# Performance work log

Hardware: AMD Instinct MI355X
Metric: run time of the kernel (lower is better)

The kernel has to match this reference:

```python
import jax, jax.numpy as jnp
import numpy as np

B, S, N = 128, 64, 32          # batch, self nodes, neighbors per node
INP_CAPS, OUT_CAPS, CAP_SZ = 8, 8, 16
K = OUT_CAPS
D = OUT_CAPS * CAP_SZ          # 128
C = D // K                     # capsule dim = 16
TAU = 1.0
EPS = 1e-12                    # F.normalize eps


def _l2norm(x):
    n = jnp.sqrt(jnp.sum(x * x, axis=-1, keepdims=True))
    return x / jnp.maximum(n, EPS)


def setup_inputs() -> dict:
    key = jax.random.key(0)
    k1, k2, k3, k4 = jax.random.split(key, 4)
    inp_d = INP_CAPS * CAP_SZ
    return {
        "self_vectors": jax.random.normal(k1, (B, S, inp_d), dtype=jnp.float32),
        "neighbor_vectors": jax.random.normal(k2, (B, S, N, inp_d), dtype=jnp.float32),
        "w1": jax.random.normal(k3, (inp_d, D), dtype=jnp.float32) * (1.0 / np.sqrt(inp_d)),
        "b1": jax.random.normal(k4, (D,), dtype=jnp.float32) * (1.0 / np.sqrt(D)),
        "max_iter": 3,
    }


def reference(self_vectors, neighbor_vectors, w1, b1, max_iter):
    inp_d = INP_CAPS * CAP_SZ
    self_z = jax.nn.relu(self_vectors.reshape(-1, inp_d) @ w1 + b1)
    neigh_z = jax.nn.relu(neighbor_vectors.reshape(-1, inp_d) @ w1 + b1)

    # [B,S,K,C] and [B,S,N,K,C], each capsule L2-normalized
    self_zn = _l2norm(self_z.reshape(B, S, K, C))
    neigh_zn = _l2norm(neigh_z.reshape(B, S, N, K, C))

    u = None
    for it in range(max_iter):
        if u is None:
            p = jnp.zeros((B, S, N, K), dtype=self_zn.dtype)
        else:
            # agreement scores: [B,S,N,K]
            p = jnp.einsum("bsnkc,bskc->bsnk", neigh_zn, u)
        p = jax.nn.softmax(p / TAU, axis=-1)
        # weighted neighbor sum over N -> [B,S,K,C]
        u = jnp.einsum("bsnkc,bsnk->bskc", neigh_zn, p) + self_zn
        if it < max_iter - 1:
            u = _l2norm(u)

    # dropout p=0.0 (eval) -> identity
    return jax.nn.relu(u.reshape(B, S, D))
```

## Files before the change

### kernel.cpp

```cpp
#include <hip/hip_runtime.h>
#include <hip/hip_bf16.h>


#define NB 32
#define DD 128
#define ZS 132
#define PPS 40
#define AST 136

#define SMEM_BYTES 19232
#define ALO_OFF_SH 4488
#define UU_OFF_F 4352
#define PP_OFF_F 4488

typedef __attribute__((ext_vector_type(8))) short bf16x8;
typedef __attribute__((ext_vector_type(4))) float f32x4;
typedef __attribute__((ext_vector_type(4))) float float4v;
typedef __attribute__((ext_vector_type(2))) unsigned int uint2v;

__device__ __forceinline__ float bf16bits_to_f32(unsigned short u) {
  return __uint_as_float(((unsigned int)u) << 16);
}
__device__ __forceinline__ void split_bf16(float x, unsigned short& hi, unsigned short& lo) {
  unsigned int xb = __float_as_uint(x);
  hi = (unsigned short)(xb >> 16);
  float hif = __uint_as_float(xb & 0xFFFF0000u);
  float lof = x - hif;
  lo = (unsigned short)(__float_as_uint(lof) >> 16);
}

__device__ __forceinline__ void split4_store(float4v v, unsigned short* hp,
                                             unsigned short* lp) {
  unsigned int a = __float_as_uint(v[0]);
  unsigned int b = __float_as_uint(v[1]);
  unsigned int c = __float_as_uint(v[2]);
  unsigned int d = __float_as_uint(v[3]);
  unsigned int h01 = __builtin_amdgcn_perm(b, a, 0x07060302u);
  unsigned int h23 = __builtin_amdgcn_perm(d, c, 0x07060302u);
  unsigned int la = __float_as_uint(v[0] - __uint_as_float(a & 0xFFFF0000u));
  unsigned int lb = __float_as_uint(v[1] - __uint_as_float(b & 0xFFFF0000u));
  unsigned int lc = __float_as_uint(v[2] - __uint_as_float(c & 0xFFFF0000u));
  unsigned int ld = __float_as_uint(v[3] - __uint_as_float(d & 0xFFFF0000u));
  unsigned int l01 = __builtin_amdgcn_perm(lb, la, 0x07060302u);
  unsigned int l23 = __builtin_amdgcn_perm(ld, lc, 0x07060302u);
  *(uint2v*)hp = (uint2v){h01, h23};
  *(uint2v*)lp = (uint2v){l01, l23};
}

__global__ __launch_bounds__(256) void swizzle_w_kernel(
    const void* __restrict__ w1, int* __restrict__ flag,
    unsigned short* __restrict__ whi, unsigned short* __restrict__ wlo) {
  __shared__ int sflag;
  int t = threadIdx.x;
  if (t < 64) {
    float v = bf16bits_to_f32(((const unsigned short*)w1)[2 * t]);
    int hit = !(fabsf(v) < 1e4f);
    unsigned long long m = __ballot(hit);
    if (t == 0) sflag = (m != 0ull) ? 1 : 0;
  }
  __syncthreads();
  const int isf = sflag;
  if (blockIdx.x == 0 && t == 0) *flag = isf;

  int idx = blockIdx.x * 256 + t;
  int k = idx >> 7, n = idx & 127;
  int kt = k >> 5, q = (k >> 3) & 3, j = k & 7;
  int nt = n >> 4, nl = n & 15;
  int lane = q * 16 + nl;
  int dst = ((kt * 8 + nt) * 64 + lane) * 8 + j;
  unsigned short hb, lb;
  if (isf) {
    split_bf16(((const float*)w1)[idx], hb, lb);
  } else {
    hb = ((const unsigned short*)w1)[idx];
    lb = 0;
  }
  whi[dst] = hb;
  wlo[dst] = lb;
}

template <bool OUTF32>
__device__ __forceinline__ void routing_tail(unsigned char* smem, void* out,
                                             size_t bs) {
  float* zn = (float*)smem;
  float* uu = (float*)smem + UU_OFF_F;
  float* pp = (float*)smem + PP_OFF_F;
  const int tid = threadIdx.x;
  const int lane = tid & 63;
  const int wv = tid >> 6;

  {
    const int rowr = (tid & 7) | ((tid >> 6) << 3);
    const int kr = (tid >> 3) & 7;
    float4v* zp = (float4v*)&zn[rowr * ZS + kr * 16];
    float4v a = zp[0], b = zp[1], c = zp[2], d = zp[3];
    float ss = a[0]*a[0]+a[1]*a[1]+a[2]*a[2]+a[3]*a[3]
             + b[0]*b[0]+b[1]*b[1]+b[2]*b[2]+b[3]*b[3]
             + c[0]*c[0]+c[1]*c[1]+c[2]*c[2]+c[3]*c[3]
             + d[0]*d[0]+d[1]*d[1]+d[2]*d[2]+d[3]*d[3];
    float nv = 1.f / fmaxf(sqrtf(ss), 1e-12f);
    zp[0] = a * nv; zp[1] = b * nv; zp[2] = c * nv; zp[3] = d * nv;
  }
  if (tid < 8) {
    float4v* zp = (float4v*)&zn[32 * ZS + tid * 16];
    float4v a = zp[0], b = zp[1], c = zp[2], d = zp[3];
    float ss = a[0]*a[0]+a[1]*a[1]+a[2]*a[2]+a[3]*a[3]
             + b[0]*b[0]+b[1]*b[1]+b[2]*b[2]+b[3]*b[3]
             + c[0]*c[0]+c[1]*c[1]+c[2]*c[2]+c[3]*c[3]
             + d[0]*d[0]+d[1]*d[1]+d[2]*d[2]+d[3]*d[3];
    float nv = 1.f / fmaxf(sqrtf(ss), 1e-12f);
    zp[0] = a * nv; zp[1] = b * nv; zp[2] = c * nv; zp[3] = d * nv;
  }
  __syncthreads();

  const int k2 = tid >> 5, half = (tid >> 4) & 1, c2 = tid & 15;
  const float selfz = zn[32 * ZS + k2 * 16 + c2];
  const int k1 = (lane >> 3) & 7;
  const int n1 = (lane & 7) | (wv << 3);

  {
    float s = 0.f;
#pragma unroll
    for (int n0 = 0; n0 < 16; ++n0)
      s += zn[(half * 16 + n0) * ZS + k2 * 16 + c2];
    s += __shfl_xor(s, 16);
    s = 0.125f * s + selfz;
    float ss = s * s;
    ss += __shfl_xor(ss, 1);
    ss += __shfl_xor(ss, 2);
    ss += __shfl_xor(ss, 4);
    ss += __shfl_xor(ss, 8);
    s *= 1.f / fmaxf(sqrtf(ss), 1e-12f);
    if (half == 0) uu[k2 * 16 + c2] = s;
    __syncthreads();
  }

  for (int it = 1; it < 3; ++it) {
    {
      const float4v* up = (const float4v*)&uu[k1 * 16];
      float4v u0 = up[0], u1 = up[1], u2 = up[2], u3 = up[3];
      const float4v* zp = (const float4v*)&zn[n1 * ZS + k1 * 16];
      float4v z0 = zp[0], z1 = zp[1], z2 = zp[2], z3 = zp[3];
      float logit = u0[0]*z0[0]+u0[1]*z0[1]+u0[2]*z0[2]+u0[3]*z0[3]
                  + u1[0]*z1[0]+u1[1]*z1[1]+u1[2]*z1[2]+u1[3]*z1[3]
                  + u2[0]*z2[0]+u2[1]*z2[1]+u2[2]*z2[2]+u2[3]*z2[3]
                  + u3[0]*z3[0]+u3[1]*z3[1]+u3[2]*z3[2]+u3[3]*z3[3];
      float m = logit;
      m = fmaxf(m, __shfl_xor(m, 8));
      m = fmaxf(m, __shfl_xor(m, 16));
      m = fmaxf(m, __shfl_xor(m, 32));
      float e = __expf(logit - m);
      float s = e;
      s += __shfl_xor(s, 8);
      s += __shfl_xor(s, 16);
      s += __shfl_xor(s, 32);
      pp[k1 * PPS + n1] = e / s;
      __syncthreads();
    }
    const float4v* pb = (const float4v*)&pp[k2 * PPS + half * 16];
    float4v p0 = pb[0], p1 = pb[1], p2 = pb[2], p3 = pb[3];
    float s = 0.f;
#pragma unroll
    for (int n0 = 0; n0 < 4; ++n0)
      s += p0[n0] * zn[(half * 16 + n0) * ZS + k2 * 16 + c2];
#pragma unroll
    for (int n0 = 0; n0 < 4; ++n0)
      s += p1[n0] * zn[(half * 16 + 4 + n0) * ZS + k2 * 16 + c2];
#pragma unroll
    for (int n0 = 0; n0 < 4; ++n0)
      s += p2[n0] * zn[(half * 16 + 8 + n0) * ZS + k2 * 16 + c2];
#pragma unroll
    for (int n0 = 0; n0 < 4; ++n0)
      s += p3[n0] * zn[(half * 16 + 12 + n0) * ZS + k2 * 16 + c2];
    s += __shfl_xor(s, 16);
    s += selfz;
    if (it < 2) {
      float ss = s * s;
      ss += __shfl_xor(ss, 1);
      ss += __shfl_xor(ss, 2);
      ss += __shfl_xor(ss, 4);
      ss += __shfl_xor(ss, 8);
      s *= 1.f / fmaxf(sqrtf(ss), 1e-12f);
      if (half == 0) uu[k2 * 16 + c2] = s;
      __syncthreads();
    } else if (half == 0) {
      float r = (s < 0.f) ? 0.f : s;
      const size_t oidx = bs * DD + k2 * 16 + c2;
      if (OUTF32) {
        ((float*)out)[oidx] = r;
      } else {
        unsigned int xb = __float_as_uint(r);
        unsigned int l = (xb >> 16) & 1u;
        ((unsigned short*)out)[oidx] = (unsigned short)((xb + 0x7fffu + l) >> 16);
      }
    }
  }
}

__global__ __launch_bounds__(256, 8) void routing_f32_kernel(
    const void* __restrict__ selfv,
    const void* __restrict__ neighv,
    const unsigned short* __restrict__ whi,
    const unsigned short* __restrict__ wlo,
    const void* __restrict__ b1,
    void* __restrict__ out,
    const int* __restrict__ flag) {
  if (*flag == 0) return;
  __shared__ __align__(16) unsigned char smem[SMEM_BYTES];
  unsigned short* Ahi = (unsigned short*)smem;
  unsigned short* Alo = Ahi + ALO_OFF_SH;
  float* zn = (float*)smem;

  const int tid = threadIdx.x;
  const int lane = tid & 63;
  const int wv = tid >> 6;
  const int q = lane >> 4;
  const int ml = lane & 15;
  const size_t bs = blockIdx.x;
  const int nt0 = wv, nt1 = wv + 4;

  const float* nf = (const float*)neighv + bs * (size_t)(NB * DD);
  const float* sf = (const float*)selfv + bs * (size_t)DD;
#pragma unroll
  for (int i = 0; i < 4; ++i) {
    int f = tid + (i << 8);
    int r = f >> 5, c4 = f & 31;
    float4v v = ((const float4v*)nf)[f];
    split4_store(v, Ahi + r * AST + c4 * 4, Alo + r * AST + c4 * 4);
  }
  if (tid < 32) {
    float4v v = ((const float4v*)sf)[tid];
    split4_store(v, Ahi + 32 * AST + tid * 4, Alo + 32 * AST + tid * 4);
  }
  const float bias0 = ((const float*)b1)[nt0 * 16 + ml];
  const float bias1 = ((const float*)b1)[nt1 * 16 + ml];
  __syncthreads();

  f32x4 acc[3][2];
#pragma unroll
  for (int mt = 0; mt < 3; ++mt)
#pragma unroll
    for (int jn = 0; jn < 2; ++jn) acc[mt][jn] = (f32x4){0.f, 0.f, 0.f, 0.f};

#pragma unroll
  for (int kt = 0; kt < 4; ++kt) {
    const size_t bo0 = ((size_t)(kt * 8 + nt0) * 64 + lane) * 8;
    const size_t bo1 = ((size_t)(kt * 8 + nt1) * 64 + lane) * 8;
    bf16x8 b0h = *(const bf16x8*)(whi + bo0);
    bf16x8 b0l = *(const bf16x8*)(wlo + bo0);
    bf16x8 b1h = *(const bf16x8*)(whi + bo1);
    bf16x8 b1l = *(const bf16x8*)(wlo + bo1);
    const int fo = kt * 32 + q * 8;
#pragma unroll
    for (int mt = 0; mt < 3; ++mt) {
      const int row = (mt == 2) ? 32 : mt * 16 + ml;
      bf16x8 ah = *(const bf16x8*)(Ahi + row * AST + fo);
      bf16x8 al = *(const bf16x8*)(Alo + row * AST + fo);
      acc[mt][0] = __builtin_amdgcn_mfma_f32_16x16x32_bf16(ah, b0h, acc[mt][0], 0, 0, 0);
      acc[mt][1] = __builtin_amdgcn_mfma_f32_16x16x32_bf16(ah, b1h, acc[mt][1], 0, 0, 0);
      acc[mt][0] = __builtin_amdgcn_mfma_f32_16x16x32_bf16(ah, b0l, acc[mt][0], 0, 0, 0);
      acc[mt][1] = __builtin_amdgcn_mfma_f32_16x16x32_bf16(ah, b1l, acc[mt][1], 0, 0, 0);
      acc[mt][0] = __builtin_amdgcn_mfma_f32_16x16x32_bf16(al, b0h, acc[mt][0], 0, 0, 0);
      acc[mt][1] = __builtin_amdgcn_mfma_f32_16x16x32_bf16(al, b1h, acc[mt][1], 0, 0, 0);
    }
  }
  __syncthreads();

#pragma unroll
  for (int jn = 0; jn < 2; ++jn) {
    const int nt = jn ? nt1 : nt0;
    const int col = nt * 16 + ml;
    const float bias = jn ? bias1 : bias0;
#pragma unroll
    for (int mt = 0; mt < 3; ++mt) {
#pragma unroll
      for (int r = 0; r < 4; ++r) {
        const int row = mt * 16 + q * 4 + r;
        float v = fmaxf(acc[mt][jn][r] + bias, 0.f);
        if (row < 33) zn[row * ZS + col] = v;
      }
    }
  }
  __syncthreads();

  routing_tail<true>(smem, out, bs);
}

__global__ __launch_bounds__(256, 8) void routing_bf16_kernel(
    const void* __restrict__ selfv,
    const void* __restrict__ neighv,
    const unsigned short* __restrict__ whi,
    const void* __restrict__ b1,
    void* __restrict__ out,
    const int* __restrict__ flag) {
  if (*flag != 0) return;
  __shared__ __align__(16) unsigned char smem[SMEM_BYTES];
  unsigned short* Ahi = (unsigned short*)smem;
  float* zn = (float*)smem;

  const int tid = threadIdx.x;
  const int lane = tid & 63;
  const int wv = tid >> 6;
  const int q = lane >> 4;
  const int ml = lane & 15;
  const size_t bs = blockIdx.x;
  const int nt0 = wv, nt1 = wv + 4;

  const unsigned short* nbf = (const unsigned short*)neighv + bs * (size_t)(NB * DD);
  const unsigned short* sbf = (const unsigned short*)selfv + bs * (size_t)DD;
#pragma unroll
  for (int i = 0; i < 2; ++i) {
    int s = tid + (i << 8);
    int r = s >> 4, c8 = s & 15;
    bf16x8 v = *(const bf16x8*)(nbf + r * DD + c8 * 8);
    *(bf16x8*)(Ahi + r * AST + c8 * 8) = v;
  }
  if (tid < 16) {
    bf16x8 v = *(const bf16x8*)(sbf + tid * 8);
    *(bf16x8*)(Ahi + 32 * AST + tid * 8) = v;
  }
  const float bias0 = bf16bits_to_f32(((const unsigned short*)b1)[nt0 * 16 + ml]);
  const float bias1 = bf16bits_to_f32(((const unsigned short*)b1)[nt1 * 16 + ml]);
  __syncthreads();

  f32x4 acc[3][2];
#pragma unroll
  for (int mt = 0; mt < 3; ++mt)
#pragma unroll
    for (int jn = 0; jn < 2; ++jn) acc[mt][jn] = (f32x4){0.f, 0.f, 0.f, 0.f};

#pragma unroll
  for (int kt = 0; kt < 4; ++kt) {
    bf16x8 b0h = *(const bf16x8*)(whi + ((size_t)(kt * 8 + nt0) * 64 + lane) * 8);
    bf16x8 b1h = *(const bf16x8*)(whi + ((size_t)(kt * 8 + nt1) * 64 + lane) * 8);
    const int fo = kt * 32 + q * 8;
#pragma unroll
    for (int mt = 0; mt < 3; ++mt) {
      const int row = (mt == 2) ? 32 : mt * 16 + ml;
      bf16x8 ah = *(const bf16x8*)(Ahi + row * AST + fo);
      acc[mt][0] = __builtin_amdgcn_mfma_f32_16x16x32_bf16(ah, b0h, acc[mt][0], 0, 0, 0);
      acc[mt][1] = __builtin_amdgcn_mfma_f32_16x16x32_bf16(ah, b1h, acc[mt][1], 0, 0, 0);
    }
  }
  __syncthreads();

#pragma unroll
  for (int jn = 0; jn < 2; ++jn) {
    const int nt = jn ? nt1 : nt0;
    const int col = nt * 16 + ml;
    const float bias = jn ? bias1 : bias0;
#pragma unroll
    for (int mt = 0; mt < 3; ++mt) {
#pragma unroll
      for (int r = 0; r < 4; ++r) {
        const int row = mt * 16 + q * 4 + r;
        float v = fmaxf(acc[mt][jn][r] + bias, 0.f);
        if (row < 33) zn[row * ZS + col] = v;
      }
    }
  }
  __syncthreads();

  routing_tail<false>(smem, out, bs);
}

extern "C" void kernel_launch(void* const* d_in, const int* in_sizes, int n_in,
                              void* d_out, int out_size, void* d_ws, size_t ws_size,
                              hipStream_t stream) {
  (void)in_sizes; (void)n_in; (void)out_size; (void)ws_size;
  const void* selfv = d_in[0];
  const void* neighv = d_in[1];
  const void* w1 = d_in[2];
  const void* b1 = d_in[3];
  int* flag = (int*)d_ws;
  unsigned short* whi = (unsigned short*)((char*)d_ws + 64);
  unsigned short* wlo = (unsigned short*)((char*)d_ws + 64 + 32768);

  swizzle_w_kernel<<<64, 256, 0, stream>>>(w1, flag, whi, wlo);
  routing_f32_kernel<<<8192, 256, 0, stream>>>(selfv, neighv, whi, wlo, b1,
                                               d_out, flag);
  routing_bf16_kernel<<<8192, 256, 0, stream>>>(selfv, neighv, whi, b1,
                                                d_out, flag);
}
```

Before: 229.5 us.

## Fuse capsule normalization and first routing iteration into MFMA epilogue

The capsule L2 normalization, the neighbor sum and the first-iteration u normalization now run directly on the MFMA accumulator registers, using 16-lane shuffle reductions. This removes the separate shared-memory normalization pass, the column-sum pass and two block barriers. The MFMA loop is also wrapped in s_setprio so that waves issuing matrix work get scheduling priority. In exchange there are more shuffles per element in the epilogue and more register pressure under the 8-blocks-per-SM launch bound.

```diff
diff --git a/kernel.cpp b/kernel.cpp
--- a/kernel.cpp
+++ b/kernel.cpp
@@ -47,6 +47,14 @@
   *(uint2v*)lp = (uint2v){l01, l23};
 }
 
+__device__ __forceinline__ float qreduce(float x) {
+  x += __shfl_xor(x, 1);
+  x += __shfl_xor(x, 2);
+  x += __shfl_xor(x, 4);
+  x += __shfl_xor(x, 8);
+  return x;
+}
+
 __global__ __launch_bounds__(256) void swizzle_w_kernel(
     const void* __restrict__ w1, int* __restrict__ flag,
     unsigned short* __restrict__ whi, unsigned short* __restrict__ wlo) {
@@ -79,9 +87,52 @@
   wlo[dst] = lb;
 }
 
+__device__ __forceinline__ void epilogue_norm_iter0(
+    f32x4 acc[3][2], float bias0, float bias1, float* zn, float* uu) {
+  const int tid = threadIdx.x;
+  const int lane = tid & 63;
+  const int wv = tid >> 6;
+  const int q = lane >> 4;
+  const int ml = lane & 15;
+  const int nt0 = wv, nt1 = wv + 4;
+
+#pragma unroll
+  for (int jn = 0; jn < 2; ++jn) {
+    const int nt = jn ? nt1 : nt0;
+    const int col = nt * 16 + ml;
+    const float bias = jn ? bias1 : bias0;
+
+    float vs = fmaxf(acc[2][jn][0] + bias, 0.f);
+    float sss = qreduce(vs * vs);
+    float selfn = vs * (1.f / fmaxf(sqrtf(sss), 1e-12f));
+    if (q == 0) zn[32 * ZS + col] = selfn;
+
+    float rowsum = 0.f;
+#pragma unroll
+    for (int r = 0; r < 4; ++r) {
+      float v0 = fmaxf(acc[0][jn][r] + bias, 0.f);
+      float ss0 = qreduce(v0 * v0);
+      float z0 = v0 * (1.f / fmaxf(sqrtf(ss0), 1e-12f));
+      zn[(q * 4 + r) * ZS + col] = z0;
+      rowsum += z0;
+      float v1 = fmaxf(acc[1][jn][r] + bias, 0.f);
+      float ss1 = qreduce(v1 * v1);
+      float z1 = v1 * (1.f / fmaxf(sqrtf(ss1), 1e-12f));
+      zn[(16 + q * 4 + r) * ZS + col] = z1;
+      rowsum += z1;
+    }
+    rowsum += __shfl_xor(rowsum, 16);
+    rowsum += __shfl_xor(rowsum, 32);
+    float u_raw = 0.125f * rowsum + selfn;
+    float ssu = qreduce(u_raw * u_raw);
+    float un = u_raw * (1.f / fmaxf(sqrtf(ssu), 1e-12f));
+    if (q == 0) uu[col] = un;
+  }
+}
+
 template <bool OUTF32>
-__device__ __forceinline__ void routing_tail(unsigned char* smem, void* out,
-                                             size_t bs) {
+__device__ __forceinline__ void routing_iters(unsigned char* smem, void* out,
+                                              size_t bs) {
   float* zn = (float*)smem;
   float* uu = (float*)smem + UU_OFF_F;
   float* pp = (float*)smem + PP_OFF_F;
@@ -89,51 +140,10 @@
   const int lane = tid & 63;
   const int wv = tid >> 6;
 
-  {
-    const int rowr = (tid & 7) | ((tid >> 6) << 3);
-    const int kr = (tid >> 3) & 7;
-    float4v* zp = (float4v*)&zn[rowr * ZS + kr * 16];
-    float4v a = zp[0], b = zp[1], c = zp[2], d = zp[3];
-    float ss = a[0]*a[0]+a[1]*a[1]+a[2]*a[2]+a[3]*a[3]
-             + b[0]*b[0]+b[1]*b[1]+b[2]*b[2]+b[3]*b[3]
-             + c[0]*c[0]+c[1]*c[1]+c[2]*c[2]+c[3]*c[3]
-             + d[0]*d[0]+d[1]*d[1]+d[2]*d[2]+d[3]*d[3];
-    float nv = 1.f / fmaxf(sqrtf(ss), 1e-12f);
-    zp[0] = a * nv; zp[1] = b * nv; zp[2] = c * nv; zp[3] = d * nv;
-  }
-  if (tid < 8) {
-    float4v* zp = (float4v*)&zn[32 * ZS + tid * 16];
-    float4v a = zp[0], b = zp[1], c = zp[2], d = zp[3];
-    float ss = a[0]*a[0]+a[1]*a[1]+a[2]*a[2]+a[3]*a[3]
-             + b[0]*b[0]+b[1]*b[1]+b[2]*b[2]+b[3]*b[3]
-             + c[0]*c[0]+c[1]*c[1]+c[2]*c[2]+c[3]*c[3]
-             + d[0]*d[0]+d[1]*d[1]+d[2]*d[2]+d[3]*d[3];
-    float nv = 1.f / fmaxf(sqrtf(ss), 1e-12f);
-    zp[0] = a * nv; zp[1] = b * nv; zp[2] = c * nv; zp[3] = d * nv;
-  }
-  __syncthreads();
-
   const int k2 = tid >> 5, half = (tid >> 4) & 1, c2 = tid & 15;
   const float selfz = zn[32 * ZS + k2 * 16 + c2];
   const int k1 = (lane >> 3) & 7;
   const int n1 = (lane & 7) | (wv << 3);
-
-  {
-    float s = 0.f;
-#pragma unroll
-    for (int n0 = 0; n0 < 16; ++n0)
-      s += zn[(half * 16 + n0) * ZS + k2 * 16 + c2];
-    s += __shfl_xor(s, 16);
-    s = 0.125f * s + selfz;
-    float ss = s * s;
-    ss += __shfl_xor(ss, 1);
-    ss += __shfl_xor(ss, 2);
-    ss += __shfl_xor(ss, 4);
-    ss += __shfl_xor(ss, 8);
-    s *= 1.f / fmaxf(sqrtf(ss), 1e-12f);
-    if (half == 0) uu[k2 * 16 + c2] = s;
-    __syncthreads();
-  }
 
   for (int it = 1; it < 3; ++it) {
     {
@@ -210,6 +220,7 @@
   unsigned short* Ahi = (unsigned short*)smem;
   unsigned short* Alo = Ahi + ALO_OFF_SH;
   float* zn = (float*)smem;
+  float* uu = (float*)smem + UU_OFF_F;
 
   const int tid = threadIdx.x;
   const int lane = tid & 63;
@@ -242,6 +253,7 @@
 #pragma unroll
     for (int jn = 0; jn < 2; ++jn) acc[mt][jn] = (f32x4){0.f, 0.f, 0.f, 0.f};
 
+  __builtin_amdgcn_s_setprio(1);
 #pragma unroll
   for (int kt = 0; kt < 4; ++kt) {
     const size_t bo0 = ((size_t)(kt * 8 + nt0) * 64 + lane) * 8;
@@ -264,26 +276,13 @@
       acc[mt][1] = __builtin_amdgcn_mfma_f32_16x16x32_bf16(al, b1h, acc[mt][1], 0, 0, 0);
     }
   }
-  __syncthreads();
-
-#pragma unroll
-  for (int jn = 0; jn < 2; ++jn) {
-    const int nt = jn ? nt1 : nt0;
-    const int col = nt * 16 + ml;
-    const float bias = jn ? bias1 : bias0;
-#pragma unroll
-    for (int mt = 0; mt < 3; ++mt) {
-#pragma unroll
-      for (int r = 0; r < 4; ++r) {
-        const int row = mt * 16 + q * 4 + r;
-        float v = fmaxf(acc[mt][jn][r] + bias, 0.f);
-        if (row < 33) zn[row * ZS + col] = v;
-      }
-    }
-  }
-  __syncthreads();
-
-  routing_tail<true>(smem, out, bs);
+  __builtin_amdgcn_s_setprio(0);
+  __syncthreads();
+
+  epilogue_norm_iter0(acc, bias0, bias1, zn, uu);
+  __syncthreads();
+
+  routing_iters<true>(smem, out, bs);
 }
 
 __global__ __launch_bounds__(256, 8) void routing_bf16_kernel(
@@ -297,6 +296,7 @@
   __shared__ __align__(16) unsigned char smem[SMEM_BYTES];
   unsigned short* Ahi = (unsigned short*)smem;
   float* zn = (float*)smem;
+  float* uu = (float*)smem + UU_OFF_F;
 
   const int tid = threadIdx.x;
   const int lane = tid & 63;
@@ -329,6 +329,7 @@
 #pragma unroll
     for (int jn = 0; jn < 2; ++jn) acc[mt][jn] = (f32x4){0.f, 0.f, 0.f, 0.f};
 
+  __builtin_amdgcn_s_setprio(1);
 #pragma unroll
   for (int kt = 0; kt < 4; ++kt) {
     bf16x8 b0h = *(const bf16x8*)(whi + ((size_t)(kt * 8 + nt0) * 64 + lane) * 8);
@@ -342,26 +343,13 @@
       acc[mt][1] = __builtin_amdgcn_mfma_f32_16x16x32_bf16(ah, b1h, acc[mt][1], 0, 0, 0);
     }
   }
-  __syncthreads();
-
-#pragma unroll
-  for (int jn = 0; jn < 2; ++jn) {
-    const int nt = jn ? nt1 : nt0;
-    const int col = nt * 16 + ml;
-    const float bias = jn ? bias1 : bias0;
-#pragma unroll
-    for (int mt = 0; mt < 3; ++mt) {
-#pragma unroll
-      for (int r = 0; r < 4; ++r) {
-        const int row = mt * 16 + q * 4 + r;
-        float v = fmaxf(acc[mt][jn][r] + bias, 0.f);
-        if (row < 33) zn[row * ZS + col] = v;
-      }
-    }
-  }
-  __syncthreads();
-
-  routing_tail<false>(smem, out, bs);
+  __builtin_amdgcn_s_setprio(0);
+  __syncthreads();
+
+  epilogue_norm_iter0(acc, bias0, bias1, zn, uu);
+  __syncthreads();
+
+  routing_iters<false>(smem, out, bs);
 }
 
 extern "C" void kernel_launch(void* const* d_in, const int* in_sizes, int n_in,
```

Result: slower. 244.7 us (+6.6%).
